# Kernel tuning notes

Measured on AMD Instinct MI355X. Metric: run time of the kernel, lower is better.

Reference implementation:

```python
import jax, jax.numpy as jnp
import numpy as np

DIM, HEADS, WS, SHIFT, HID = 256, 8, 7, 3, 1024
N = WS * WS

def _rel_index():
    coords = np.stack(np.meshgrid(np.arange(WS), np.arange(WS), indexing='ij')).reshape(2, -1)
    rel = (coords[:, :, None] - coords[:, None, :]).transpose(1, 2, 0)
    rel[:, :, 0] += WS - 1
    rel[:, :, 1] += WS - 1
    rel[:, :, 0] *= 2 * WS - 1
    return rel.sum(-1)  # [N, N] int

def _attn_mask(hp, wp):
    img = np.zeros((hp, wp))
    slices = (slice(0, -WS), slice(-WS, -SHIFT), slice(-SHIFT, None))
    cnt = 0
    for hs in slices:
        for ws_ in slices:
            img[hs, ws_] = cnt
            cnt += 1
    mw = img.reshape(hp // WS, WS, wp // WS, WS).transpose(0, 2, 1, 3).reshape(-1, N)
    am = mw[:, None, :] - mw[:, :, None]  # [nw, N, N]
    return np.where(am != 0, -100.0, 0.0).astype(np.float32)

def _ln(t, g, b):
    mu = t.mean(-1, keepdims=True)
    var = ((t - mu) ** 2).mean(-1, keepdims=True)
    return (t - mu) / jnp.sqrt(var + 1e-5) * g + b

def setup_inputs() -> dict:
    key = jax.random.key(0)
    ks = jax.random.split(key, 16)
    b, h, w = 16, 112, 112
    p = lambda k, shape: jax.random.normal(k, shape, dtype=jnp.float32) * 0.02
    return {
        'x': jax.random.normal(ks[0], (b, h * w, DIM), dtype=jnp.float32),
        'norm1_w': jnp.ones((DIM,), jnp.float32), 'norm1_b': jnp.zeros((DIM,), jnp.float32),
        'qkv_w': p(ks[1], (DIM, 3 * DIM)), 'qkv_b': jnp.zeros((3 * DIM,), jnp.float32),
        'proj_w': p(ks[2], (DIM, DIM)), 'proj_b': jnp.zeros((DIM,), jnp.float32),
        'bias_table': p(ks[3], ((2 * WS - 1) * (2 * WS - 1), HEADS)),
        'norm2_w': jnp.ones((DIM,), jnp.float32), 'norm2_b': jnp.zeros((DIM,), jnp.float32),
        'fc1_w': p(ks[4], (DIM, HID)), 'fc1_b': jnp.zeros((HID,), jnp.float32),
        'fc2_w': p(ks[5], (HID, DIM)), 'fc2_b': jnp.zeros((DIM,), jnp.float32),
        'h': h, 'w': w,
    }

def reference(x, norm1_w, norm1_b, qkv_w, qkv_b, proj_w, proj_b, bias_table,
              norm2_w, norm2_b, fc1_w, fc1_b, fc2_w, fc2_b, h, w):
    b, l, c = x.shape
    hd = c // HEADS
    shortcut = x
    xn = _ln(x, norm1_w, norm1_b).reshape(b, h, w, c)
    pad_b, pad_r = (-h) % WS, (-w) % WS
    if pad_b or pad_r:
        xn = jnp.pad(xn, ((0, 0), (0, pad_b), (0, pad_r), (0, 0)))
    hp, wp = h + pad_b, w + pad_r
    xs = jnp.roll(xn, (-SHIFT, -SHIFT), (1, 2))
    # window partition -> [B_, N, c]
    win = xs.reshape(b, hp // WS, WS, wp // WS, WS, c).transpose(0, 1, 3, 2, 4, 5).reshape(-1, N, c)
    qkv = (win @ qkv_w + qkv_b).reshape(-1, N, 3, HEADS, hd).transpose(2, 0, 3, 1, 4)
    q, k, v = qkv[0] * (hd ** -0.5), qkv[1], qkv[2]
    attn = jnp.einsum('bhnd,bhmd->bhnm', q, k)  # [B_, H, N, N]
    rpb = bias_table[jnp.asarray(_rel_index().reshape(-1))].reshape(N, N, HEADS).transpose(2, 0, 1)
    attn = attn + rpb[None]
    mask = jnp.asarray(_attn_mask(hp, wp))  # [nw, N, N]
    nw = mask.shape[0]
    attn = (attn.reshape(b, nw, HEADS, N, N) + mask[None, :, None]).reshape(-1, HEADS, N, N)
    attn = jax.nn.softmax(attn, axis=-1)
    out = jnp.einsum('bhnm,bhmd->bhnd', attn, v).transpose(0, 2, 1, 3).reshape(-1, N, c)
    out = out @ proj_w + proj_b
    # window reverse
    out = out.reshape(b, hp // WS, wp // WS, WS, WS, c).transpose(0, 1, 3, 2, 4, 5).reshape(b, hp, wp, c)
    out = jnp.roll(out, (SHIFT, SHIFT), (1, 2))[:, :h, :w].reshape(b, h * w, c)
    x = shortcut + out
    x = x + (jax.nn.gelu(_ln(x, norm2_w, norm2_b) @ fc1_w + fc1_b, approximate=False) @ fc2_w + fc2_b)
    return x
```

## Files before the change

### kernel.cpp

```cpp
#include <hip/hip_runtime.h>
#include <stdint.h>
#include <math.h>

#define DIMC   256
#define NHEADS 8
#define WSZ    7
#define NTOK   49
#define HIDN   1024
#define IMGS   112
#define BATCH  16
#define NWIN   4096
#define MTOT   200704

using frag_ab = __attribute__((ext_vector_type(8))) short;
using frag_cd = __attribute__((ext_vector_type(4))) float;

__device__ __forceinline__ float b2f(ushort u) {
    union { float f; uint32_t i; } c; c.i = ((uint32_t)u) << 16; return c.f;
}
__device__ __forceinline__ ushort f2b(float f) {
    union { float f; uint32_t i; } c; c.f = f;
    uint32_t r = c.i + 0x7fffu + ((c.i >> 16) & 1u);
    return (ushort)(r >> 16);
}

__device__ __forceinline__ void gld16(const ushort* g, ushort* l) {
    __builtin_amdgcn_global_load_lds(
        (const __attribute__((address_space(1))) void*)g,
        (__attribute__((address_space(3))) void*)l, 16, 0, 0);
}

__global__ void detect_kernel(const uint32_t* __restrict__ w, int* __restrict__ flag) {
    if (threadIdx.x == 0 && blockIdx.x == 0)
        *flag = (w[0] == 0x3F800000u) ? 1 : 0;
}

__global__ void cvt_kernel(const void* __restrict__ src, ushort* __restrict__ dst,
                           int n, const int* __restrict__ dflag) {
    int i = blockIdx.x * 256 + threadIdx.x;
    if (i < n)
        dst[i] = (*dflag) ? f2b(((const float*)src)[i]) : ((const ushort*)src)[i];
}

__global__ void transpose_cvt(const void* __restrict__ src, ushort* __restrict__ dst,
                              int K, int N, const int* __restrict__ dflag) {
    int idx = blockIdx.x * 256 + threadIdx.x;
    if (idx < K * N) {
        int k = idx / N, n = idx - k * N;
        ushort v = (*dflag) ? f2b(((const float*)src)[idx]) : ((const ushort*)src)[idx];
        dst[n * K + k] = v;
    }
}

__global__ __launch_bounds__(256)
void zero_vpad(ushort* __restrict__ vt) {
    int idx = blockIdx.x * 256 + threadIdx.x;
    float4 z = {0.f, 0.f, 0.f, 0.f};
    *(float4*)(vt + ((size_t)(idx >> 1) << 6) + 48 + (idx & 1) * 8) = z;
}

template <bool REMAP>
__global__ __launch_bounds__(256)
void ln_kernel(const void* __restrict__ xin, const ushort* __restrict__ g,
               const ushort* __restrict__ bt, ushort* __restrict__ out,
               const int* __restrict__ dflag) {
    int gw = (blockIdx.x * 256 + threadIdx.x) >> 6;
    int lane = threadIdx.x & 63;
    if (gw >= MTOT) return;
    float v0, v1, v2, v3;
    if constexpr (REMAP) {
        if (*dflag) {
            float4 xv = *(const float4*)((const float*)xin + (size_t)gw * DIMC + lane * 4);
            v0 = xv.x; v1 = xv.y; v2 = xv.z; v3 = xv.w;
        } else {
            ushort4 xv = *(const ushort4*)((const ushort*)xin + (size_t)gw * DIMC + lane * 4);
            v0 = b2f(xv.x); v1 = b2f(xv.y); v2 = b2f(xv.z); v3 = b2f(xv.w);
        }
    } else {
        ushort4 xv = *(const ushort4*)((const ushort*)xin + (size_t)gw * DIMC + lane * 4);
        v0 = b2f(xv.x); v1 = b2f(xv.y); v2 = b2f(xv.z); v3 = b2f(xv.w);
    }
    float s = v0 + v1 + v2 + v3;
#pragma unroll
    for (int off = 32; off; off >>= 1) s += __shfl_xor(s, off);
    float mean = s * (1.f / 256.f);
    float d0 = v0 - mean, d1 = v1 - mean, d2 = v2 - mean, d3 = v3 - mean;
    float q = d0 * d0 + d1 * d1 + d2 * d2 + d3 * d3;
#pragma unroll
    for (int off = 32; off; off >>= 1) q += __shfl_xor(q, off);
    float inv = rsqrtf(q * (1.f / 256.f) + 1e-5f);
    ushort4 gv = *(const ushort4*)(g + lane * 4);
    ushort4 bv = *(const ushort4*)(bt + lane * 4);
    ushort4 o;
    o.x = f2b(d0 * inv * b2f(gv.x) + b2f(bv.x));
    o.y = f2b(d1 * inv * b2f(gv.y) + b2f(bv.y));
    o.z = f2b(d2 * inv * b2f(gv.z) + b2f(bv.z));
    o.w = f2b(d3 * inv * b2f(gv.w) + b2f(bv.w));
    size_t orow;
    if constexpr (REMAP) {
        int b = gw / 12544, sres = gw - b * 12544;
        int row = sres / IMGS, col = sres - row * IMGS;
        int r = row - 3; if (r < 0) r += IMGS;
        int c = col - 3; if (c < 0) c += IMGS;
        int wh = r / WSZ, tr = r - wh * WSZ;
        int ww = c / WSZ, tc = c - ww * WSZ;
        orow = (size_t)(((b * 16 + wh) * 16 + ww)) * NTOK + (tr * WSZ + tc);
    } else {
        orow = gw;
    }
    *(ushort4*)(out + orow * DIMC + lane * 4) = o;
}

template <int MODE>
__global__ __launch_bounds__(256)
void gemm_bt(const ushort* __restrict__ A, const ushort* __restrict__ Bt,
             const ushort* __restrict__ bias, void* __restrict__ outv,
             const void* __restrict__ add, int M, int N, int K,
             const int* __restrict__ dflag) {
    __shared__ __align__(16) ushort As[128 * 32];
    __shared__ __align__(16) ushort Bs[128 * 32];
    const int t = threadIdx.x;
    const int lane = t & 63, wave = t >> 6;
    const int wr = (wave >> 1) * 64, wc = (wave & 1) * 64;
    const int lrow = lane & 15, lq8 = (lane >> 4) * 8;
    const int bm = blockIdx.x * 128, bn = blockIdx.y * 128;
    const int arow = t >> 2, acol = (t & 3) * 8;

    int isf32 = 0;
    if constexpr (MODE == 1) isf32 = *dflag;

    frag_cd acc[4][4];
#pragma unroll
    for (int i = 0; i < 4; i++)
#pragma unroll
        for (int j = 0; j < 4; j++) acc[i][j] = (frag_cd){0.f, 0.f, 0.f, 0.f};

    const ushort* Ag0 = A + (size_t)(bm + arow) * K + acol;
    const ushort* Ag1 = Ag0 + (size_t)64 * K;
    const ushort* Bg0 = Bt + (size_t)(bn + arow) * K + acol;
    const ushort* Bg1 = Bg0 + (size_t)64 * K;
    ushort* Al0 = &As[arow * 32 + acol];
    ushort* Al1 = &As[(arow + 64) * 32 + acol];
    ushort* Bl0 = &Bs[arow * 32 + acol];
    ushort* Bl1 = &Bs[(arow + 64) * 32 + acol];

    for (int kk = 0; kk < K; kk += 32) {
        __syncthreads();
        gld16(Ag0 + kk, Al0);
        gld16(Ag1 + kk, Al1);
        gld16(Bg0 + kk, Bl0);
        gld16(Bg1 + kk, Bl1);
        __syncthreads();
        frag_ab af[4], bfr[4];
#pragma unroll
        for (int i = 0; i < 4; i++)
            af[i] = *(const frag_ab*)&As[(wr + i * 16 + lrow) * 32 + lq8];
#pragma unroll
        for (int j = 0; j < 4; j++)
            bfr[j] = *(const frag_ab*)&Bs[(wc + j * 16 + lrow) * 32 + lq8];
#pragma unroll
        for (int i = 0; i < 4; i++)
#pragma unroll
            for (int j = 0; j < 4; j++)
                acc[i][j] = __builtin_amdgcn_mfma_f32_16x16x32_bf16(
                    af[i], bfr[j], acc[i][j], 0, 0, 0);
    }

    ushort* out = (ushort*)outv;
    float*  outf = (float*)outv;

#pragma unroll
    for (int i = 0; i < 4; i++) {
#pragma unroll
        for (int rg = 0; rg < 4; rg++) {
            const int gm = bm + wr + i * 16 + (lane >> 4) * 4 + rg;
            int win = 0, tok = 0;
            size_t rowbase = 0;
            if constexpr (MODE == 0) {
                win = gm / 49; tok = gm - win * 49;
            } else if constexpr (MODE == 1) {
                win = gm / 49; tok = gm - win * 49;
                int b = win >> 8, wh = (win >> 4) & 15, ww = win & 15;
                int tr = tok / 7, tc = tok - tr * 7;
                int r = wh * 7 + tr + 3; if (r >= IMGS) r -= IMGS;
                int c = ww * 7 + tc + 3; if (c >= IMGS) c -= IMGS;
                rowbase = ((size_t)b * 12544 + r * IMGS + c) * DIMC;
            } else {
                rowbase = (size_t)gm * N;
            }
#pragma unroll
            for (int j = 0; j < 4; j++) {
                const int gn = bn + wc + j * 16 + lrow;
                float v = acc[i][j][rg] + b2f(bias[gn]);
                if constexpr (MODE == 0) {
                    int part = gn >> 8, hd = (gn >> 5) & 7, dd = gn & 31;
                    if (part == 0) v *= 0.17677669529663687f;
                    if (part == 2) {
                        out[(size_t)2 * MTOT * DIMC +
                            (((size_t)win * NHEADS + hd) * 32 + dd) * 64 + tok] = f2b(v);
                    } else {
                        out[(size_t)part * ((size_t)MTOT * DIMC) +
                            (((size_t)win * NHEADS + hd) * NTOK + tok) * 32 + dd] = f2b(v);
                    }
                } else if constexpr (MODE == 1) {
                    float r = isf32 ? ((const float*)add)[rowbase + gn]
                                    : b2f(((const ushort*)add)[rowbase + gn]);
                    v += r;
                    out[rowbase + gn] = f2b(v);
                } else if constexpr (MODE == 2) {
                    v = 0.5f * v * (1.f + erff(v * 0.70710678118654752f));
                    out[rowbase + gn] = f2b(v);
                } else {
                    v += b2f(((const ushort*)add)[rowbase + gn]);
                    outf[rowbase + gn] = v;
                }
            }
        }
    }
}

__global__ __launch_bounds__(256)
void attn_kernel(const ushort* __restrict__ qb, const ushort* __restrict__ kb,
                 const ushort* __restrict__ vtb, const ushort* __restrict__ btab,
                 ushort* __restrict__ out) {
    __shared__ __align__(16) ushort Pl[4][2][16][72];
    __shared__ float bbs[4][172];
    const int t = threadIdx.x;
    const int wv = t >> 6, l = t & 63;
    const int lo = l & 15, hi = l >> 4;
    const int gw = blockIdx.x * 4 + wv;
    const int win = gw >> 3, hd = gw & 7;
    const int wh = (win >> 4) & 15, ww = win & 15;

    for (int idx = l; idx < 169; idx += 64)
        bbs[wv][idx] = b2f(btab[idx * NHEADS + hd]);

    const ushort* qp = qb  + (size_t)gw * (NTOK * 32);
    const ushort* kp = kb  + (size_t)gw * (NTOK * 32);
    const ushort* vp = vtb + (size_t)gw * (32 * 64);

    frag_ab af[4], bfr[4];
#pragma unroll
    for (int i = 0; i < 4; i++) {
        af[i]  = *(const frag_ab*)(qp + (i * 16 + lo) * 32 + hi * 8);
        bfr[i] = *(const frag_ab*)(kp + (i * 16 + lo) * 32 + hi * 8);
    }
    frag_ab vf[2][2];
#pragma unroll
    for (int j = 0; j < 2; j++)
#pragma unroll
        for (int kk = 0; kk < 2; kk++)
            vf[j][kk] = *(const frag_ab*)(vp + (j * 16 + lo) * 64 + kk * 32 + hi * 8);

    frag_cd S[4][4];
#pragma unroll
    for (int i = 0; i < 4; i++)
#pragma unroll
        for (int j = 0; j < 4; j++) S[i][j] = (frag_cd){0.f, 0.f, 0.f, 0.f};
#pragma unroll
    for (int i = 0; i < 4; i++)
#pragma unroll
        for (int j = 0; j < 4; j++)
            S[i][j] = __builtin_amdgcn_mfma_f32_16x16x32_bf16(af[i], bfr[j], S[i][j], 0, 0, 0);

    int cy[4], cx[4], rvj[4], rhj[4];
#pragma unroll
    for (int j = 0; j < 4; j++) {
        int c = j * 16 + lo;
        int y = (c * 9363) >> 16;
        cy[j] = y; cx[j] = c - y * 7;
        rvj[j] = (wh < 15) ? 0 : ((cy[j] < 4) ? 1 : 2);
        rhj[j] = (ww < 15) ? 0 : ((cx[j] < 4) ? 1 : 2);
    }

    frag_cd o[4][2];
#pragma unroll
    for (int i = 0; i < 4; i++)
#pragma unroll
        for (int j = 0; j < 2; j++) o[i][j] = (frag_cd){0.f, 0.f, 0.f, 0.f};

#pragma unroll
    for (int i = 0; i < 4; i++) {
        const int cur = i & 1;
#pragma unroll
        for (int rg = 0; rg < 4; rg++) {
            int r = i * 16 + hi * 4 + rg;
            int rr = (r < NTOK) ? r : 0;
            int yi = (rr * 9363) >> 16, xi = rr - yi * 7;
            int rvi = (wh < 15) ? 0 : ((yi < 4) ? 1 : 2);
            int rhi = (ww < 15) ? 0 : ((xi < 4) ? 1 : 2);
            float xs[4];
#pragma unroll
            for (int j = 0; j < 4; j++) {
                bool valid = (j < 3) | (lo == 0);
                float v = S[i][j][rg]
                        + bbs[wv][(yi - cy[j] + 6) * 13 + (xi - cx[j] + 6)];
                v = (rvi != rvj[j] || rhi != rhj[j]) ? v - 100.f : v;
                xs[j] = valid ? v : -1e30f;
            }
            float m = fmaxf(fmaxf(xs[0], xs[1]), fmaxf(xs[2], xs[3]));
#pragma unroll
            for (int off = 8; off; off >>= 1) m = fmaxf(m, __shfl_xor(m, off));
            float e0 = __expf(xs[0] - m);
            float e1 = __expf(xs[1] - m);
            float e2 = __expf(xs[2] - m);
            float e3 = __expf(xs[3] - m);
            float sum = e0 + e1 + e2 + e3;
#pragma unroll
            for (int off = 8; off; off >>= 1) sum += __shfl_xor(sum, off);
            float inv = 1.f / sum;
            int rl = hi * 4 + rg;
            int sw = ((rl >> 3) & 1) << 4;
            ushort* prow = &Pl[wv][cur][rl][0];
            prow[(lo +  0) ^ sw] = f2b(e0 * inv);
            prow[(lo + 16) ^ sw] = f2b(e1 * inv);
            prow[(lo + 32) ^ sw] = f2b(e2 * inv);
            prow[(lo + 48) ^ sw] = f2b(e3 * inv);
        }
        int swr = ((lo >> 3) & 1) << 4;
        frag_ab pa0 = *(const frag_ab*)&Pl[wv][cur][lo][(      hi * 8) ^ swr];
        frag_ab pa1 = *(const frag_ab*)&Pl[wv][cur][lo][(32 + hi * 8) ^ swr];
#pragma unroll
        for (int j = 0; j < 2; j++) {
            o[i][j] = __builtin_amdgcn_mfma_f32_16x16x32_bf16(pa0, vf[j][0], o[i][j], 0, 0, 0);
            o[i][j] = __builtin_amdgcn_mfma_f32_16x16x32_bf16(pa1, vf[j][1], o[i][j], 0, 0, 0);
        }
    }

#pragma unroll
    for (int i = 0; i < 4; i++)
#pragma unroll
        for (int rg = 0; rg < 4; rg++) {
            int r = i * 16 + hi * 4 + rg;
            if (r < NTOK) {
                size_t ob = ((size_t)win * NTOK + r) * DIMC + hd * 32;
                out[ob + lo]      = f2b(o[i][0][rg]);
                out[ob + 16 + lo] = f2b(o[i][1][rg]);
            }
        }
}

extern "C" void kernel_launch(void* const* d_in, const int* in_sizes, int n_in,
                              void* d_out, int out_size, void* d_ws, size_t ws_size,
                              hipStream_t stream) {
    (void)in_sizes; (void)n_in; (void)out_size;
    const void* x        = d_in[0];
    const void* norm1_w  = d_in[1];
    const void* norm1_b  = d_in[2];
    const void* qkv_w    = d_in[3];
    const void* qkv_b    = d_in[4];
    const void* proj_w   = d_in[5];
    const void* proj_b   = d_in[6];
    const void* btab     = d_in[7];
    const void* norm2_w  = d_in[8];
    const void* norm2_b  = d_in[9];
    const void* fc1_w    = d_in[10];
    const void* fc1_b    = d_in[11];
    const void* fc2_w    = d_in[12];
    const void* fc2_b    = d_in[13];

    const size_t szA   = (size_t)MTOT * DIMC * 2;
    const size_t szBIG = (size_t)MTOT * HIDN * 2;
    const size_t szWT  = (size_t)(768 * 256 + 256 * 256 + 256 * 1024 + 1024 * 256) * 2;
    const size_t szSV  = 16384;
    const size_t need  = szSV + szA * 2 + szBIG + szWT;
    if (ws_size < need) return;

    char* ws = (char*)d_ws;
    ushort* sv    = (ushort*)ws;
    ushort* svN1w = sv + 0;
    ushort* svN1b = sv + 256;
    ushort* svQKb = sv + 512;
    ushort* svPJb = sv + 1280;
    ushort* svN2w = sv + 1536;
    ushort* svN2b = sv + 1792;
    ushort* svF1b = sv + 2048;
    ushort* svF2b = sv + 3072;
    ushort* svBT  = sv + 3328;
    int*    dflag = (int*)(ws + szSV - 256);

    char* big = ws + szSV;
    ushort* bufA   = (ushort*)big;
    ushort* bufBIG = (ushort*)(big + szA);
    ushort* bufQ   = bufBIG;
    ushort* bufK   = bufBIG + (size_t)MTOT * DIMC;
    ushort* bufV   = bufBIG + (size_t)2 * MTOT * DIMC;
    ushort* bufX1  = (ushort*)(big + szA + szBIG);
    ushort* qkvT   = (ushort*)(big + szA + szBIG + szA);
    ushort* projT  = qkvT + 768 * 256;
    ushort* fc1T   = projT + 256 * 256;
    ushort* fc2T   = fc1T + 256 * 1024;

    detect_kernel<<<1, 64, 0, stream>>>((const uint32_t*)norm1_w, dflag);

    zero_vpad<<<8192, 256, 0, stream>>>(bufV);

    cvt_kernel<<<1, 256, 0, stream>>>(norm1_w, svN1w, 256, dflag);
    cvt_kernel<<<1, 256, 0, stream>>>(norm1_b, svN1b, 256, dflag);
    cvt_kernel<<<3, 256, 0, stream>>>(qkv_b,  svQKb, 768, dflag);
    cvt_kernel<<<1, 256, 0, stream>>>(proj_b, svPJb, 256, dflag);
    cvt_kernel<<<1, 256, 0, stream>>>(norm2_w, svN2w, 256, dflag);
    cvt_kernel<<<1, 256, 0, stream>>>(norm2_b, svN2b, 256, dflag);
    cvt_kernel<<<4, 256, 0, stream>>>(fc1_b,  svF1b, 1024, dflag);
    cvt_kernel<<<1, 256, 0, stream>>>(fc2_b,  svF2b, 256, dflag);
    cvt_kernel<<<6, 256, 0, stream>>>(btab,   svBT, 1352, dflag);

    transpose_cvt<<<(768 * 256 + 255) / 256, 256, 0, stream>>>(qkv_w, qkvT, 256, 768, dflag);
    transpose_cvt<<<(256 * 256 + 255) / 256, 256, 0, stream>>>(proj_w, projT, 256, 256, dflag);
    transpose_cvt<<<(256 * 1024 + 255) / 256, 256, 0, stream>>>(fc1_w, fc1T, 256, 1024, dflag);
    transpose_cvt<<<(1024 * 256 + 255) / 256, 256, 0, stream>>>(fc2_w, fc2T, 1024, 256, dflag);

    ln_kernel<true><<<MTOT / 4, 256, 0, stream>>>(x, svN1w, svN1b, bufA, dflag);

    gemm_bt<0><<<dim3(MTOT / 128, 768 / 128), 256, 0, stream>>>(
        bufA, qkvT, svQKb, bufBIG, nullptr, MTOT, 768, 256, dflag);

    attn_kernel<<<NWIN * NHEADS / 4, 256, 0, stream>>>(bufQ, bufK, bufV, svBT, bufA);

    gemm_bt<1><<<dim3(MTOT / 128, 256 / 128), 256, 0, stream>>>(
        bufA, projT, svPJb, bufX1, x, MTOT, 256, 256, dflag);

    ln_kernel<false><<<MTOT / 4, 256, 0, stream>>>(bufX1, svN2w, svN2b, bufA, dflag);

    gemm_bt<2><<<dim3(MTOT / 128, 1024 / 128), 256, 0, stream>>>(
        bufA, fc1T, svF1b, bufBIG, nullptr, MTOT, 1024, 256, dflag);

    gemm_bt<3><<<dim3(MTOT / 128, 256 / 128), 256, 0, stream>>>(
        bufBIG, fc2T, svF2b, d_out, bufX1, MTOT, 256, 1024, dflag);
}
```

Before: 1.653 ms.

## Double-buffer GEMM LDS tiles and swap grid order so N-tiles share A rows

The bf16 MFMA GEMM now keeps two LDS buffers for A and B. The next K-slice is loaded while the current one feeds the MFMAs, and the two barriers per iteration become one. The grid is also transposed so that blocks with the same M-tile run next to each other, which should improve L2 reuse of the A rows. The cost is double the LDS (32 KB per block), which may lower occupancy.

```diff
diff --git a/kernel.cpp b/kernel.cpp
--- a/kernel.cpp
+++ b/kernel.cpp
@@ -117,13 +117,13 @@
              const ushort* __restrict__ bias, void* __restrict__ outv,
              const void* __restrict__ add, int M, int N, int K,
              const int* __restrict__ dflag) {
-    __shared__ __align__(16) ushort As[128 * 32];
-    __shared__ __align__(16) ushort Bs[128 * 32];
+    __shared__ __align__(16) ushort As[2][128 * 32];
+    __shared__ __align__(16) ushort Bs[2][128 * 32];
     const int t = threadIdx.x;
     const int lane = t & 63, wave = t >> 6;
     const int wr = (wave >> 1) * 64, wc = (wave & 1) * 64;
     const int lrow = lane & 15, lq8 = (lane >> 4) * 8;
-    const int bm = blockIdx.x * 128, bn = blockIdx.y * 128;
+    const int bm = blockIdx.y * 128, bn = blockIdx.x * 128;
     const int arow = t >> 2, acol = (t & 3) * 8;
 
     int isf32 = 0;
@@ -139,31 +139,39 @@
     const ushort* Ag1 = Ag0 + (size_t)64 * K;
     const ushort* Bg0 = Bt + (size_t)(bn + arow) * K + acol;
     const ushort* Bg1 = Bg0 + (size_t)64 * K;
-    ushort* Al0 = &As[arow * 32 + acol];
-    ushort* Al1 = &As[(arow + 64) * 32 + acol];
-    ushort* Bl0 = &Bs[arow * 32 + acol];
-    ushort* Bl1 = &Bs[(arow + 64) * 32 + acol];
-
+    const int lofs0 = arow * 32 + acol;
+    const int lofs1 = (arow + 64) * 32 + acol;
+
+    gld16(Ag0, &As[0][lofs0]);
+    gld16(Ag1, &As[0][lofs1]);
+    gld16(Bg0, &Bs[0][lofs0]);
+    gld16(Bg1, &Bs[0][lofs1]);
+    __syncthreads();
+
+    int cur = 0;
     for (int kk = 0; kk < K; kk += 32) {
-        __syncthreads();
-        gld16(Ag0 + kk, Al0);
-        gld16(Ag1 + kk, Al1);
-        gld16(Bg0 + kk, Bl0);
-        gld16(Bg1 + kk, Bl1);
-        __syncthreads();
+        const int nxt = cur ^ 1;
+        if (kk + 32 < K) {
+            gld16(Ag0 + kk + 32, &As[nxt][lofs0]);
+            gld16(Ag1 + kk + 32, &As[nxt][lofs1]);
+            gld16(Bg0 + kk + 32, &Bs[nxt][lofs0]);
+            gld16(Bg1 + kk + 32, &Bs[nxt][lofs1]);
+        }
         frag_ab af[4], bfr[4];
 #pragma unroll
         for (int i = 0; i < 4; i++)
-            af[i] = *(const frag_ab*)&As[(wr + i * 16 + lrow) * 32 + lq8];
+            af[i] = *(const frag_ab*)&As[cur][(wr + i * 16 + lrow) * 32 + lq8];
 #pragma unroll
         for (int j = 0; j < 4; j++)
-            bfr[j] = *(const frag_ab*)&Bs[(wc + j * 16 + lrow) * 32 + lq8];
+            bfr[j] = *(const frag_ab*)&Bs[cur][(wc + j * 16 + lrow) * 32 + lq8];
 #pragma unroll
         for (int i = 0; i < 4; i++)
 #pragma unroll
             for (int j = 0; j < 4; j++)
                 acc[i][j] = __builtin_amdgcn_mfma_f32_16x16x32_bf16(
                     af[i], bfr[j], acc[i][j], 0, 0, 0);
+        __syncthreads();
+        cur = nxt;
     }
 
     ushort* out = (ushort*)outv;
@@ -412,19 +420,19 @@
 
     ln_kernel<true><<<MTOT / 4, 256, 0, stream>>>(x, svN1w, svN1b, bufA, dflag);
 
-    gemm_bt<0><<<dim3(MTOT / 128, 768 / 128), 256, 0, stream>>>(
+    gemm_bt<0><<<dim3(768 / 128, MTOT / 128), 256, 0, stream>>>(
         bufA, qkvT, svQKb, bufBIG, nullptr, MTOT, 768, 256, dflag);
 
     attn_kernel<<<NWIN * NHEADS / 4, 256, 0, stream>>>(bufQ, bufK, bufV, svBT, bufA);
 
-    gemm_bt<1><<<dim3(MTOT / 128, 256 / 128), 256, 0, stream>>>(
+    gemm_bt<1><<<dim3(256 / 128, MTOT / 128), 256, 0, stream>>>(
         bufA, projT, svPJb, bufX1, x, MTOT, 256, 256, dflag);
 
     ln_kernel<false><<<MTOT / 4, 256, 0, stream>>>(bufX1, svN2w, svN2b, bufA, dflag);
 
-    gemm_bt<2><<<dim3(MTOT / 128, 1024 / 128), 256, 0, stream>>>(
+    gemm_bt<2><<<dim3(1024 / 128, MTOT / 128), 256, 0, stream>>>(
         bufA, fc1T, svF1b, bufBIG, nullptr, MTOT, 1024, 256, dflag);
 
-    gemm_bt<3><<<dim3(MTOT / 128, 256 / 128), 256, 0, stream>>>(
+    gemm_bt<3><<<dim3(256 / 128, MTOT / 128), 256, 0, stream>>>(
         bufBIG, fc2T, svF2b, d_out, bufX1, MTOT, 256, 1024, dflag);
 }
```

Result: faster. 1.561 ms (-5.6%).
